# Performance work log

Hardware: AMD Instinct MI355X
Metric: run time of the kernel (lower is better)

Reference implementation:

```python
import jax, jax.numpy as jnp
import numpy as np

EPS = 1e-5

def conv2d(x, w, stride=1, padding=0, bias=None):
    out = jax.lax.conv_general_dilated(
        x, w, (stride, stride), [(padding, padding), (padding, padding)],
        dimension_numbers=('NCHW', 'OIHW', 'NCHW'))
    if bias is not None:
        out = out + bias[None, :, None, None]
    return out

def bn_relu(x, gamma, beta, mean, var):
    scale = gamma / jnp.sqrt(var + EPS)
    return jax.nn.relu(x * scale[None, :, None, None]
                       + (beta - mean * scale)[None, :, None, None])

def deform_conv(x, wp, bp, wc, ks, pad, stride):
    # Canonical DeformConv2d (v1, modulation=False) from pytorch-deform-conv-v2.
    b, c, H, W = x.shape
    N = ks * ks
    offset = conv2d(x, wp, stride=stride, padding=1, bias=bp)        # (b,2N,h,w)
    h, w = offset.shape[2], offset.shape[3]
    xp = jnp.pad(x, ((0, 0), (0, 0), (pad, pad), (pad, pad)))        # zero_padding
    Hp, Wp = H + 2 * pad, W + 2 * pad
    off = offset.transpose(0, 2, 3, 1)                               # (b,h,w,2N)
    rng = jnp.arange(-(ks - 1) // 2, (ks - 1) // 2 + 1, dtype=x.dtype)
    pnx, pny = jnp.meshgrid(rng, rng, indexing='ij')
    pnx, pny = pnx.reshape(-1), pny.reshape(-1)                      # (N,)
    p0x = jnp.arange(1, h * stride + 1, stride, dtype=x.dtype)       # torch starts at 1
    p0y = jnp.arange(1, w * stride + 1, stride, dtype=x.dtype)
    px = p0x[None, :, None, None] + pnx[None, None, None, :] + off[..., :N]  # (b,h,w,N)
    py = p0y[None, None, :, None] + pny[None, None, None, :] + off[..., N:]
    qx0 = jnp.floor(jax.lax.stop_gradient(px))
    qy0 = jnp.floor(jax.lax.stop_gradient(py))
    qx0c = jnp.clip(qx0, 0, Hp - 1).astype(jnp.int32)
    qx1c = jnp.clip(qx0 + 1, 0, Hp - 1).astype(jnp.int32)
    qy0c = jnp.clip(qy0, 0, Wp - 1).astype(jnp.int32)
    qy1c = jnp.clip(qy0 + 1, 0, Wp - 1).astype(jnp.int32)
    pxc = jnp.clip(px, 0, Hp - 1)
    pyc = jnp.clip(py, 0, Wp - 1)
    fx0 = qx0c.astype(x.dtype); fx1 = qx1c.astype(x.dtype)
    fy0 = qy0c.astype(x.dtype); fy1 = qy1c.astype(x.dtype)
    g_lt = (1 + (fx0 - pxc)) * (1 + (fy0 - pyc))
    g_rb = (1 - (fx1 - pxc)) * (1 - (fy1 - pyc))
    g_lb = (1 + (fx0 - pxc)) * (1 - (fy1 - pyc))
    g_rt = (1 - (fx1 - pxc)) * (1 + (fy0 - pyc))
    xf = xp.reshape(b, c, Hp * Wp)
    def gather(qx, qy):
        idx = (qx * Wp + qy).reshape(b, 1, h * w * N)
        return jnp.take_along_axis(xf, idx, axis=2).reshape(b, c, h, w, N)
    x_off = (g_lt[:, None] * gather(qx0c, qy0c)
             + g_rb[:, None] * gather(qx1c, qy1c)
             + g_lb[:, None] * gather(qx0c, qy1c)
             + g_rt[:, None] * gather(qx1c, qy0c))                   # (b,c,h,w,N)
    # stride=ks conv over the reshaped (h*ks, w*ks) map == einsum over sample slot n
    return jnp.einsum('bchwn,ocn->bohw', x_off, wc.reshape(wc.shape[0], c, N))

def setup_inputs() -> dict:
    key = jax.random.key(0)
    ks = iter(jax.random.split(key, 40))
    def nrm(shape, scale):
        return jax.random.normal(next(ks), shape, dtype=jnp.float32) * scale
    def he(shape):  # fan_in = prod of all but first dim
        return nrm(shape, float(np.sqrt(2.0 / np.prod(shape[1:]))))
    def bn(c):
        return (jnp.ones((c,), jnp.float32) + nrm((c,), 0.05),  # gamma
                nrm((c,), 0.05),                                 # beta
                nrm((c,), 0.1),                                  # running mean
                jax.random.uniform(next(ks), (c,), jnp.float32, 0.5, 1.5))  # var
    inp = {'x': jax.random.normal(next(ks), (256, 3, 32, 32), dtype=jnp.float32)}
    inp['w1'] = he((32, 3, 3, 3)); inp['b1'] = nrm((32,), 0.01)
    inp['g1'], inp['be1'], inp['m1'], inp['v1'] = bn(32)
    inp['wp2'] = nrm((18, 32, 3, 3), 0.01); inp['bp2'] = nrm((18,), 0.001)
    inp['wc2'] = he((64, 32, 3, 3))
    inp['g2'], inp['be2'], inp['m2'], inp['v2'] = bn(64)
    inp['wp3'] = nrm((18, 64, 3, 3), 0.01); inp['bp3'] = nrm((18,), 0.001)
    inp['wc3'] = he((128, 64, 3, 3))
    inp['g3'], inp['be3'], inp['m3'], inp['v3'] = bn(128)
    inp['wp4'] = nrm((18, 128, 3, 3), 0.01); inp['bp4'] = nrm((18,), 0.001)
    inp['wc4'] = he((128, 128, 3, 3))
    inp['g4'], inp['be4'], inp['m4'], inp['v4'] = bn(128)
    inp['wcls'] = nrm((100, 128), float(1.0 / np.sqrt(128)))
    inp['bcls'] = nrm((100,), 0.01)
    return inp

def reference(x, w1, b1, g1, be1, m1, v1,
              wp2, bp2, wc2, g2, be2, m2, v2,
              wp3, bp3, wc3, g3, be3, m3, v3,
              wp4, bp4, wc4, g4, be4, m4, v4,
              wcls, bcls):
    h = bn_relu(conv2d(x, w1, stride=1, padding=1, bias=b1), g1, be1, m1, v1)   # (b,32,32,32)
    h = bn_relu(deform_conv(h, wp2, bp2, wc2, 3, 1, 2), g2, be2, m2, v2)        # (b,64,16,16)
    h = bn_relu(deform_conv(h, wp3, bp3, wc3, 3, 1, 1), g3, be3, m3, v3)        # (b,128,16,16)
    h = bn_relu(deform_conv(h, wp4, bp4, wc4, 3, 1, 2), g4, be4, m4, v4)        # (b,128,8,8)
    h = jnp.mean(h, axis=(2, 3))                                                # avg_pool2d(8) -> (b,128)
    return h @ wcls.T + bcls[None, :]
```

## Files before the change

### kernel.cpp

```cpp
#include <hip/hip_runtime.h>
#include <math.h>

#define BN_EPS 1e-5f

typedef __attribute__((ext_vector_type(4))) float f4;
typedef __attribute__((ext_vector_type(4))) int i4v;
typedef __attribute__((ext_vector_type(8))) short short8;
typedef __attribute__((ext_vector_type(4))) float f32x4;

__device__ inline unsigned short f2bf(float f) {
    unsigned int u = __builtin_bit_cast(unsigned int, f);
    return (unsigned short)((u + 0x7FFFu + ((u >> 16) & 1u)) >> 16);
}
__device__ inline float blo(int u) { return __builtin_bit_cast(float, (int)(u << 16)); }
__device__ inline float bhi(int u) { return __builtin_bit_cast(float, (int)(u & 0xffff0000)); }
__device__ inline int pkbf_fast(float hi, float lo) {
    unsigned uh = __builtin_bit_cast(unsigned, hi) + 0x8000u;
    unsigned ul = __builtin_bit_cast(unsigned, lo) + 0x8000u;
    return (int)__builtin_amdgcn_perm(uh, ul, 0x07060302u);
}

struct CvtSeg { const float* src; unsigned short* dst; int oreal, c, kpad, end; };
struct CvtArgs { CvtSeg s[7]; };

__global__ __launch_bounds__(256)
void cvt_all(CvtArgs a)
{
    int idx = blockIdx.x * 256 + threadIdx.x;
    int base = 0;
    #pragma unroll
    for (int i = 0; i < 7; ++i) {
        if (idx < a.s[i].end) {
            int local = idx - base;
            int kpad = a.s[i].kpad, c = a.s[i].c;
            int o = local / kpad, k = local - o * kpad;
            unsigned short val = 0;
            if (o < a.s[i].oreal && k < 9 * c) {
                int n = k / c, cc = k - n * c;
                val = f2bf(a.s[i].src[(o * c + cc) * 9 + n]);
            }
            a.s[i].dst[local] = val;
            return;
        }
        base = a.s[i].end;
    }
}

__global__ __launch_bounds__(256)
void conv1_tile(const float* __restrict__ x, const unsigned short* __restrict__ wq,
                const float* __restrict__ bias, const float* __restrict__ g,
                const float* __restrict__ be, const float* __restrict__ m,
                const float* __restrict__ v, unsigned short* __restrict__ out)
{
    __shared__ __align__(16) float img[3072];
    __shared__ __align__(16) unsigned short wt[32 * 40];
    __shared__ float scb[32], shb[32];
    const int tid = threadIdx.x;
    const int b = blockIdx.x >> 2;
    const int qtr = blockIdx.x & 3;
    if (tid < 32) {
        float sc = g[tid] * rsqrtf(v[tid] + BN_EPS);
        scb[tid] = sc;
        shb[tid] = be[tid] - m[tid] * sc + bias[tid] * sc;
    }
    *(ushort4*)&wt[(tid >> 3) * 40 + (tid & 7) * 4] =
        *(const ushort4*)(wq + (tid >> 3) * 32 + (tid & 7) * 4);
    const float* xb = x + (size_t)b * 3072;
    #pragma unroll
    for (int r = 0; r < 3; ++r) {
        int idx = r * 256 + tid;
        *(f4*)&img[idx * 4] = *(const f4*)(xb + idx * 4);
    }
    __syncthreads();
    const int wid = tid >> 6, lane = tid & 63, quad = lane >> 4, m16 = lane & 15;
    short8 af0 = *(const short8*)&wt[m16 * 40 + quad * 8];
    short8 af1 = *(const short8*)&wt[(16 + m16) * 40 + quad * 8];
    #pragma unroll
    for (int it = 0; it < 4; ++it) {
        int pix = qtr * 256 + it * 64 + wid * 16 + m16;
        int i = pix >> 5, j = pix & 31;
        short8 bfrag;
        #pragma unroll
        for (int jj = 0; jj < 8; ++jj) {
            int k = quad * 8 + jj;
            float val = 0.f;
            if (k < 27) {
                int n = k / 3, c = k - n * 3;
                int u = i - 1 + n / 3, vv = j - 1 + n % 3;
                if (u >= 0 && u < 32 && vv >= 0 && vv < 32)
                    val = img[c * 1024 + u * 32 + vv];
            }
            bfrag[jj] = (short)f2bf(val);
        }
        f32x4 a0 = {0.f,0.f,0.f,0.f}, a1 = {0.f,0.f,0.f,0.f};
        a0 = __builtin_amdgcn_mfma_f32_16x16x32_bf16(af0, bfrag, a0, 0, 0, 0);
        a1 = __builtin_amdgcn_mfma_f32_16x16x32_bf16(af1, bfrag, a1, 0, 0, 0);
        unsigned short* op = out + ((size_t)b * 1024 + pix) * 32;
        ushort4 s0, s1;
        #pragma unroll
        for (int rr = 0; rr < 4; ++rr) {
            int o0 = quad * 4 + rr, o1 = 16 + quad * 4 + rr;
            ((unsigned short*)&s0)[rr] = f2bf(fmaxf(fmaf(a0[rr], scb[o0], shb[o0]), 0.f));
            ((unsigned short*)&s1)[rr] = f2bf(fmaxf(fmaf(a1[rr], scb[o1], shb[o1]), 0.f));
        }
        *(ushort4*)(op + quad * 4) = s0;
        *(ushort4*)(op + 16 + quad * 4) = s1;
    }
}

template<int C, int OREAL, int OPAD, int H, int W, int OH, int OW, int S, int MTILE>
__global__ __launch_bounds__(256, 3)
void dconv_fused(const unsigned short* __restrict__ xact,
                 const unsigned short* __restrict__ wp, const float* __restrict__ bp,
                 const unsigned short* __restrict__ wc,
                 const float* __restrict__ g, const float* __restrict__ be,
                 const float* __restrict__ m, const float* __restrict__ v,
                 unsigned short* __restrict__ out)
{
    constexpr int K = C * 9;
    constexpr int KCH = C / 32;
    constexpr int OT = OPAD / 64;
    constexpr int ST = MTILE / 16;
    constexpr int PWP = MTILE / 2;
    constexpr int STP = PWP / 16;
    constexpr int CP = C + 8;
    constexpr int GL = C / 8;
    constexpr int NGRP = 256 / GL;
    constexpr int NT = MTILE / NGRP;
    constexpr int OHW = OH * OW;
    constexpr int HWC = H * W * C;
    constexpr int Hp = H + 2, Wpp = W + 2;
    static_assert(MTILE % NGRP == 0 && OPAD % 64 == 0, "tiling");

    __shared__ __align__(16) unsigned short xo[2][MTILE * CP];
    __shared__ __align__(16) i4v tab_i[MTILE][9];
    __shared__ __align__(16) f4  tab_w[MTILE][9];
    __shared__ int tab_o[MTILE][9];
    __shared__ int tab_m[MTILE][9];
    __shared__ float off_lds[MTILE][20];
    __shared__ int imgb[MTILE];
    __shared__ float scb[OPAD], shb[OPAD];

    const int tid = threadIdx.x;
    const int p0 = blockIdx.x * MTILE;

    if (tid < MTILE) imgb[tid] = ((p0 + tid) / OHW) * HWC;
    for (int o = tid; o < OREAL; o += 256) {
        float sc = g[o] * rsqrtf(v[o] + BN_EPS);
        scb[o] = sc;
        shb[o] = be[o] - m[o] * sc;
    }
    for (int e = tid; e < MTILE * 9; e += 256) {
        int lp = e / 9, n = e % 9;
        int p = p0 + lp;
        int rem = p % OHW;
        int i = rem / OW, j = rem % OW;
        int u = i * S - 1 + n / 3, vv = j * S - 1 + n % 3;
        bool ok = (u >= 0 && u < H && vv >= 0 && vv < W);
        tab_o[lp][n] = ok ? (u * W + vv) * C : 0;
        tab_m[lp][n] = ok ? -1 : 0;
    }
    __syncthreads();

    const int gl = tid % GL, grp = tid / GL;
    const int wid = tid >> 6, lane = tid & 63, quad = lane >> 4, m16 = lane & 15;

    {
        const int ogp = wid & 1, pgp = wid >> 1;
        const int obp = ogp * 16;
        const int pbp = pgp * PWP;
        i4v Tp[NT];
        auto issueA = [&](int n) {
            #pragma unroll
            for (int it = 0; it < NT; ++it) {
                const int pix = it * NGRP + grp;
                Tp[it] = *(const i4v*)(xact + imgb[pix] + gl * 8 + tab_o[pix][n]);
            }
        };
        auto commitA = [&](int n, int buf) {
            #pragma unroll
            for (int it = 0; it < NT; ++it) {
                const int pix = it * NGRP + grp;
                int mask = tab_m[pix][n];
                i4v R;
                #pragma unroll
                for (int e2 = 0; e2 < 4; ++e2) R[e2] = Tp[it][e2] & mask;
                *(i4v*)&xo[buf][pix * CP + gl * 8] = R;
            }
        };
        auto loadWp = [&](int n, short8* wf) {
            #pragma unroll
            for (int ch = 0; ch < KCH; ++ch)
                wf[ch] = *(const short8*)(wp + (size_t)(obp + m16) * K
                                          + n * C + ch * 32 + quad * 8);
        };
        f32x4 accp[STP];
        #pragma unroll
        for (int st = 0; st < STP; ++st) accp[st] = (f32x4){0.f, 0.f, 0.f, 0.f};
        short8 wfA[KCH], wfB[KCH];
        issueA(0);
        loadWp(0, wfA);
        commitA(0, 0);
        __syncthreads();
        for (int n = 0; n < 9; ++n) {
            const int cur = n & 1;
            if (n < 8) { issueA(n + 1); loadWp(n + 1, wfB); }
            #pragma unroll
            for (int ch = 0; ch < KCH; ++ch)
                #pragma unroll
                for (int st = 0; st < STP; ++st) {
                    short8 bf = *(const short8*)&xo[cur][(pbp + st * 16 + m16) * CP
                                                        + ch * 32 + quad * 8];
                    accp[st] = __builtin_amdgcn_mfma_f32_16x16x32_bf16(
                        wfA[ch], bf, accp[st], 0, 0, 0);
                }
            if (n < 8) {
                commitA(n + 1, cur ^ 1);
                #pragma unroll
                for (int ch = 0; ch < KCH; ++ch) wfA[ch] = wfB[ch];
            }
            __syncthreads();
        }
        #pragma unroll
        for (int st = 0; st < STP; ++st) {
            int pix = pbp + st * 16 + m16;
            #pragma unroll
            for (int rr = 0; rr < 4; ++rr) {
                int o = obp + quad * 4 + rr;
                if (o < 18) off_lds[pix][o] = accp[st][rr] + bp[o];
            }
        }
    }
    __syncthreads();

    for (int e = tid; e < MTILE * 9; e += 256) {
        int lp = e / 9, n = e % 9;
        int p = p0 + lp;
        int rem = p % OHW;
        int i = rem / OW, j = rem % OW;
        float ox = off_lds[lp][n];
        float oy = off_lds[lp][9 + n];
        float px = (float)(i * S + n / 3) + ox;
        float py = (float)(j * S + n % 3) + oy;
        int qx0 = (int)floorf(px), qy0 = (int)floorf(py);
        int x0 = min(max(qx0, 0), Hp - 1), x1 = min(max(qx0 + 1, 0), Hp - 1);
        int y0 = min(max(qy0, 0), Wpp - 1), y1 = min(max(qy0 + 1, 0), Wpp - 1);
        float pxc = fminf(fmaxf(px, 0.f), (float)(Hp - 1));
        float pyc = fminf(fmaxf(py, 0.f), (float)(Wpp - 1));
        float gx0 = 1.f + ((float)x0 - pxc), gx1 = 1.f - ((float)x1 - pxc);
        float gy0 = 1.f + ((float)y0 - pyc), gy1 = 1.f - ((float)y1 - pyc);
        int u0 = x0 - 1, u1 = x1 - 1, v0 = y0 - 1, v1 = y1 - 1;
        bool k0 = (u0 >= 0 && u0 < H && v0 >= 0 && v0 < W);
        bool k1 = (u1 >= 0 && u1 < H && v1 >= 0 && v1 < W);
        bool k2 = (u0 >= 0 && u0 < H && v1 >= 0 && v1 < W);
        bool k3 = (u1 >= 0 && u1 < H && v0 >= 0 && v0 < W);
        i4v ti; f4 tw;
        ti[0] = k0 ? (u0 * W + v0) * C : 0;  tw[0] = k0 ? gx0 * gy0 : 0.f;
        ti[1] = k1 ? (u1 * W + v1) * C : 0;  tw[1] = k1 ? gx1 * gy1 : 0.f;
        ti[2] = k2 ? (u0 * W + v1) * C : 0;  tw[2] = k2 ? gx0 * gy1 : 0.f;
        ti[3] = k3 ? (u1 * W + v0) * C : 0;  tw[3] = k3 ? gx1 * gy0 : 0.f;
        tab_i[lp][n] = ti;
        tab_w[lp][n] = tw;
    }
    __syncthreads();

    {
        const int obase = wid * OT * 16;
        i4v T[NT][4];
        auto issueC = [&](int n) {
            #pragma unroll
            for (int it = 0; it < NT; ++it) {
                const int pix = it * NGRP + grp;
                const unsigned short* xb = xact + imgb[pix] + gl * 8;
                i4v ti = tab_i[pix][n];
                T[it][0] = *(const i4v*)(xb + ti[0]);
                T[it][1] = *(const i4v*)(xb + ti[1]);
                T[it][2] = *(const i4v*)(xb + ti[2]);
                T[it][3] = *(const i4v*)(xb + ti[3]);
            }
        };
        auto commitC = [&](int n, int buf) {
            #pragma unroll
            for (int it = 0; it < NT; ++it) {
                const int pix = it * NGRP + grp;
                f4 tw = tab_w[pix][n];
                i4v R;
                #pragma unroll
                for (int e2 = 0; e2 < 4; ++e2) {
                    float lo = tw[0] * blo(T[it][0][e2]);
                    lo = fmaf(tw[1], blo(T[it][1][e2]), lo);
                    lo = fmaf(tw[2], blo(T[it][2][e2]), lo);
                    lo = fmaf(tw[3], blo(T[it][3][e2]), lo);
                    float hi = tw[0] * bhi(T[it][0][e2]);
                    hi = fmaf(tw[1], bhi(T[it][1][e2]), hi);
                    hi = fmaf(tw[2], bhi(T[it][2][e2]), hi);
                    hi = fmaf(tw[3], bhi(T[it][3][e2]), hi);
                    R[e2] = pkbf_fast(hi, lo);
                }
                *(i4v*)&xo[buf][pix * CP + gl * 8] = R;
            }
        };
        auto loadWc = [&](int n, short8 (*wf)[OT]) {
            #pragma unroll
            for (int ch = 0; ch < KCH; ++ch)
                #pragma unroll
                for (int t = 0; t < OT; ++t)
                    wf[ch][t] = *(const short8*)(wc + (size_t)(obase + t * 16 + m16) * K
                                                 + n * C + ch * 32 + quad * 8);
        };

        f32x4 acc[ST][OT];
        #pragma unroll
        for (int st = 0; st < ST; ++st)
            #pragma unroll
            for (int t = 0; t < OT; ++t) acc[st][t] = (f32x4){0.f, 0.f, 0.f, 0.f};

        short8 wfA[KCH][OT], wfB[KCH][OT];
        issueC(0);
        loadWc(0, wfA);
        commitC(0, 0);
        __syncthreads();

        for (int n = 0; n < 9; ++n) {
            const int cur = n & 1;
            if (n < 8) {
                issueC(n + 1);
                loadWc(n + 1, wfB);
            }
            #pragma unroll
            for (int ch = 0; ch < KCH; ++ch)
                #pragma unroll
                for (int st = 0; st < ST; ++st) {
                    short8 bf = *(const short8*)&xo[cur][(st * 16 + m16) * CP
                                                        + ch * 32 + quad * 8];
                    #pragma unroll
                    for (int t = 0; t < OT; ++t)
                        acc[st][t] = __builtin_amdgcn_mfma_f32_16x16x32_bf16(
                            wfA[ch][t], bf, acc[st][t], 0, 0, 0);
                }
            if (n < 8) {
                commitC(n + 1, cur ^ 1);
                #pragma unroll
                for (int ch = 0; ch < KCH; ++ch)
                    #pragma unroll
                    for (int t = 0; t < OT; ++t) wfA[ch][t] = wfB[ch][t];
            }
            __syncthreads();
        }

        #pragma unroll
        for (int st = 0; st < ST; ++st) {
            const int p = p0 + st * 16 + m16;
            #pragma unroll
            for (int t = 0; t < OT; ++t) {
                int o = obase + t * 16 + quad * 4;
                ushort4 s;
                #pragma unroll
                for (int rr = 0; rr < 4; ++rr)
                    ((unsigned short*)&s)[rr] =
                        f2bf(fmaxf(fmaf(acc[st][t][rr], scb[o + rr], shb[o + rr]), 0.f));
                *(ushort4*)(out + (size_t)p * OPAD + o) = s;
            }
        }
    }
}

__global__ __launch_bounds__(128)
void pool_fc(const unsigned short* __restrict__ h4, const float* __restrict__ wcls,
             const float* __restrict__ bcls, float* __restrict__ out)
{
    __shared__ float pool[128];
    int b = blockIdx.x;
    int tid = threadIdx.x;
    const unsigned short* src = h4 + (size_t)b * 8192;
    float s = 0.f;
    #pragma unroll
    for (int t = 0; t < 64; ++t)
        s += __builtin_bit_cast(float, (unsigned)src[t * 128 + tid] << 16);
    pool[tid] = s * (1.f / 64.f);
    __syncthreads();
    if (tid < 100) {
        float acc = bcls[tid];
        const float* wr = wcls + tid * 128;
        #pragma unroll
        for (int c = 0; c < 128; ++c) acc = fmaf(pool[c], wr[c], acc);
        out[(size_t)b * 100 + tid] = acc;
    }
}

extern "C" void kernel_launch(void* const* d_in, const int* in_sizes, int n_in,
                              void* d_out, int out_size, void* d_ws, size_t ws_size,
                              hipStream_t stream)
{
    const float* x    = (const float*)d_in[0];
    const float* w1   = (const float*)d_in[1];
    const float* b1   = (const float*)d_in[2];
    const float* g1   = (const float*)d_in[3];
    const float* be1  = (const float*)d_in[4];
    const float* m1   = (const float*)d_in[5];
    const float* v1   = (const float*)d_in[6];
    const float* wp2  = (const float*)d_in[7];
    const float* bp2  = (const float*)d_in[8];
    const float* wc2  = (const float*)d_in[9];
    const float* g2   = (const float*)d_in[10];
    const float* be2  = (const float*)d_in[11];
    const float* m2   = (const float*)d_in[12];
    const float* v2   = (const float*)d_in[13];
    const float* wp3  = (const float*)d_in[14];
    const float* bp3  = (const float*)d_in[15];
    const float* wc3  = (const float*)d_in[16];
    const float* g3   = (const float*)d_in[17];
    const float* be3  = (const float*)d_in[18];
    const float* m3   = (const float*)d_in[19];
    const float* v3   = (const float*)d_in[20];
    const float* wp4  = (const float*)d_in[21];
    const float* bp4  = (const float*)d_in[22];
    const float* wc4  = (const float*)d_in[23];
    const float* g4   = (const float*)d_in[24];
    const float* be4  = (const float*)d_in[25];
    const float* m4   = (const float*)d_in[26];
    const float* v4   = (const float*)d_in[27];
    const float* wcls = (const float*)d_in[28];
    const float* bcls = (const float*)d_in[29];
    float* out = (float*)d_out;

    unsigned short* h1 = (unsigned short*)d_ws;
    unsigned short* h2 = h1 + 8388608;
    unsigned short* h3 = h2 + 4194304;
    unsigned short* h4 = h3 + 8388608;
    unsigned short* wc2b = h4 + 2097152;
    unsigned short* wc3b = wc2b + 18432;
    unsigned short* wc4b = wc3b + 73728;
    unsigned short* wp2b = wc4b + 147456;
    unsigned short* wp3b = wp2b + 9216;
    unsigned short* wp4b = wp3b + 18432;
    unsigned short* wq1  = wp4b + 36864;
    (void)ws_size; (void)in_sizes; (void)n_in; (void)out_size;

    CvtArgs ca;
    ca.s[0] = { wc2, wc2b, 64, 32, 288, 18432 };
    ca.s[1] = { wc3, wc3b, 128, 64, 576, 92160 };
    ca.s[2] = { wc4, wc4b, 128, 128, 1152, 239616 };
    ca.s[3] = { wp2, wp2b, 18, 32, 288, 248832 };
    ca.s[4] = { wp3, wp3b, 18, 64, 576, 267264 };
    ca.s[5] = { wp4, wp4b, 18, 128, 1152, 304128 };
    ca.s[6] = { w1, wq1, 32, 3, 32, 305152 };
    cvt_all<<<1192, 256, 0, stream>>>(ca);

    conv1_tile<<<1024, 256, 0, stream>>>(x, wq1, b1, g1, be1, m1, v1, h1);

    dconv_fused<32, 64, 64, 32, 32, 16, 16, 2, 64><<<1024, 256, 0, stream>>>(
        h1, wp2b, bp2, wc2b, g2, be2, m2, v2, h2);

    dconv_fused<64, 128, 128, 16, 16, 16, 16, 1, 64><<<1024, 256, 0, stream>>>(
        h2, wp3b, bp3, wc3b, g3, be3, m3, v3, h3);

    dconv_fused<128, 128, 128, 16, 16, 8, 8, 2, 32><<<512, 256, 0, stream>>>(
        h3, wp4b, bp4, wc4b, g4, be4, m4, v4, h4);

    pool_fc<<<256, 128, 0, stream>>>(h4, wcls, bcls, out);
}
```

Measured before the change: 234.0 us.

## Compress deform-conv LDS tables to 16-bit and shrink layer-4 tile for occupancy

Gather offset tables shrink from int to ushort, and bilinear weights and predicted offsets are stored as fp16 instead of fp32. This cuts LDS use, allowing launch bounds to rise to 4 blocks per CU. The last deform layer uses MTILE 16 with twice the blocks, plus adjusted offset-conv wave mapping so small tiles still work. The risks are reduced precision in the offsets and weights (fp16 offsets near 16 lose fractional bits) and ushort offsets that must stay below 65536. With MTILE 16, two of the four waves duplicate the offset-conv work.

```diff
diff --git a/kernel.cpp b/kernel.cpp
--- a/kernel.cpp
+++ b/kernel.cpp
@@ -7,6 +7,7 @@
 typedef __attribute__((ext_vector_type(4))) int i4v;
 typedef __attribute__((ext_vector_type(8))) short short8;
 typedef __attribute__((ext_vector_type(4))) float f32x4;
+typedef _Float16 half4v __attribute__((ext_vector_type(4)));
 
 __device__ inline unsigned short f2bf(float f) {
     unsigned int u = __builtin_bit_cast(unsigned int, f);
@@ -109,7 +110,7 @@
 }
 
 template<int C, int OREAL, int OPAD, int H, int W, int OH, int OW, int S, int MTILE>
-__global__ __launch_bounds__(256, 3)
+__global__ __launch_bounds__(256, 4)
 void dconv_fused(const unsigned short* __restrict__ xact,
                  const unsigned short* __restrict__ wp, const float* __restrict__ bp,
                  const unsigned short* __restrict__ wc,
@@ -121,7 +122,7 @@
     constexpr int KCH = C / 32;
     constexpr int OT = OPAD / 64;
     constexpr int ST = MTILE / 16;
-    constexpr int PWP = MTILE / 2;
+    constexpr int PWP = (MTILE >= 32) ? MTILE / 2 : MTILE;
     constexpr int STP = PWP / 16;
     constexpr int CP = C + 8;
     constexpr int GL = C / 8;
@@ -130,14 +131,12 @@
     constexpr int OHW = OH * OW;
     constexpr int HWC = H * W * C;
     constexpr int Hp = H + 2, Wpp = W + 2;
-    static_assert(MTILE % NGRP == 0 && OPAD % 64 == 0, "tiling");
+    static_assert(MTILE % NGRP == 0 && OPAD % 64 == 0 && STP >= 1, "tiling");
 
     __shared__ __align__(16) unsigned short xo[2][MTILE * CP];
-    __shared__ __align__(16) i4v tab_i[MTILE][9];
-    __shared__ __align__(16) f4  tab_w[MTILE][9];
-    __shared__ int tab_o[MTILE][9];
-    __shared__ int tab_m[MTILE][9];
-    __shared__ float off_lds[MTILE][20];
+    __shared__ __align__(8) ushort4   tab_p[MTILE][9];
+    __shared__ __align__(8) _Float16  tab_h[MTILE][9][4];
+    __shared__ _Float16 off_lds[MTILE][20];
     __shared__ int imgb[MTILE];
     __shared__ float scb[OPAD], shb[OPAD];
 
@@ -157,8 +156,11 @@
         int i = rem / OW, j = rem % OW;
         int u = i * S - 1 + n / 3, vv = j * S - 1 + n % 3;
         bool ok = (u >= 0 && u < H && vv >= 0 && vv < W);
-        tab_o[lp][n] = ok ? (u * W + vv) * C : 0;
-        tab_m[lp][n] = ok ? -1 : 0;
+        ushort4 tp;
+        tp.x = ok ? (unsigned short)((u * W + vv) * C) : (unsigned short)0;
+        tp.y = ok ? (unsigned short)0xFFFF : (unsigned short)0;
+        tp.z = 0; tp.w = 0;
+        tab_p[lp][n] = tp;
     }
     __syncthreads();
 
@@ -166,7 +168,8 @@
     const int wid = tid >> 6, lane = tid & 63, quad = lane >> 4, m16 = lane & 15;
 
     {
-        const int ogp = wid & 1, pgp = wid >> 1;
+        const int ogp = wid & 1;
+        const int pgp = (MTILE >= 32) ? (wid >> 1) : 0;
         const int obp = ogp * 16;
         const int pbp = pgp * PWP;
         i4v Tp[NT];
@@ -174,14 +177,14 @@
             #pragma unroll
             for (int it = 0; it < NT; ++it) {
                 const int pix = it * NGRP + grp;
-                Tp[it] = *(const i4v*)(xact + imgb[pix] + gl * 8 + tab_o[pix][n]);
+                Tp[it] = *(const i4v*)(xact + imgb[pix] + gl * 8 + (int)tab_p[pix][n].x);
             }
         };
         auto commitA = [&](int n, int buf) {
             #pragma unroll
             for (int it = 0; it < NT; ++it) {
                 const int pix = it * NGRP + grp;
-                int mask = tab_m[pix][n];
+                int mask = (int)(short)tab_p[pix][n].y;
                 i4v R;
                 #pragma unroll
                 for (int e2 = 0; e2 < 4; ++e2) R[e2] = Tp[it][e2] & mask;
@@ -227,7 +230,7 @@
             #pragma unroll
             for (int rr = 0; rr < 4; ++rr) {
                 int o = obp + quad * 4 + rr;
-                if (o < 18) off_lds[pix][o] = accp[st][rr] + bp[o];
+                if (o < 18) off_lds[pix][o] = (_Float16)(accp[st][rr] + bp[o]);
             }
         }
     }
@@ -238,8 +241,8 @@
         int p = p0 + lp;
         int rem = p % OHW;
         int i = rem / OW, j = rem % OW;
-        float ox = off_lds[lp][n];
-        float oy = off_lds[lp][9 + n];
+        float ox = (float)off_lds[lp][n];
+        float oy = (float)off_lds[lp][9 + n];
         float px = (float)(i * S + n / 3) + ox;
         float py = (float)(j * S + n % 3) + oy;
         int qx0 = (int)floorf(px), qy0 = (int)floorf(py);
@@ -254,13 +257,18 @@
         bool k1 = (u1 >= 0 && u1 < H && v1 >= 0 && v1 < W);
         bool k2 = (u0 >= 0 && u0 < H && v1 >= 0 && v1 < W);
         bool k3 = (u1 >= 0 && u1 < H && v0 >= 0 && v0 < W);
-        i4v ti; f4 tw;
-        ti[0] = k0 ? (u0 * W + v0) * C : 0;  tw[0] = k0 ? gx0 * gy0 : 0.f;
-        ti[1] = k1 ? (u1 * W + v1) * C : 0;  tw[1] = k1 ? gx1 * gy1 : 0.f;
-        ti[2] = k2 ? (u0 * W + v1) * C : 0;  tw[2] = k2 ? gx0 * gy1 : 0.f;
-        ti[3] = k3 ? (u1 * W + v0) * C : 0;  tw[3] = k3 ? gx1 * gy0 : 0.f;
-        tab_i[lp][n] = ti;
-        tab_w[lp][n] = tw;
+        ushort4 tp;
+        tp.x = k0 ? (unsigned short)((u0 * W + v0) * C) : (unsigned short)0;
+        tp.y = k1 ? (unsigned short)((u1 * W + v1) * C) : (unsigned short)0;
+        tp.z = k2 ? (unsigned short)((u0 * W + v1) * C) : (unsigned short)0;
+        tp.w = k3 ? (unsigned short)((u1 * W + v0) * C) : (unsigned short)0;
+        tab_p[lp][n] = tp;
+        half4v hw;
+        hw[0] = (_Float16)(k0 ? gx0 * gy0 : 0.f);
+        hw[1] = (_Float16)(k1 ? gx1 * gy1 : 0.f);
+        hw[2] = (_Float16)(k2 ? gx0 * gy1 : 0.f);
+        hw[3] = (_Float16)(k3 ? gx1 * gy0 : 0.f);
+        *(half4v*)&tab_h[lp][n][0] = hw;
     }
     __syncthreads();
 
@@ -272,29 +280,31 @@
             for (int it = 0; it < NT; ++it) {
                 const int pix = it * NGRP + grp;
                 const unsigned short* xb = xact + imgb[pix] + gl * 8;
-                i4v ti = tab_i[pix][n];
-                T[it][0] = *(const i4v*)(xb + ti[0]);
-                T[it][1] = *(const i4v*)(xb + ti[1]);
-                T[it][2] = *(const i4v*)(xb + ti[2]);
-                T[it][3] = *(const i4v*)(xb + ti[3]);
+                ushort4 tp = tab_p[pix][n];
+                T[it][0] = *(const i4v*)(xb + tp.x);
+                T[it][1] = *(const i4v*)(xb + tp.y);
+                T[it][2] = *(const i4v*)(xb + tp.z);
+                T[it][3] = *(const i4v*)(xb + tp.w);
             }
         };
         auto commitC = [&](int n, int buf) {
             #pragma unroll
             for (int it = 0; it < NT; ++it) {
                 const int pix = it * NGRP + grp;
-                f4 tw = tab_w[pix][n];
+                half4v hw = *(const half4v*)&tab_h[pix][n][0];
+                float w0 = (float)hw[0], w1 = (float)hw[1];
+                float w2 = (float)hw[2], w3 = (float)hw[3];
                 i4v R;
                 #pragma unroll
                 for (int e2 = 0; e2 < 4; ++e2) {
-                    float lo = tw[0] * blo(T[it][0][e2]);
-                    lo = fmaf(tw[1], blo(T[it][1][e2]), lo);
-                    lo = fmaf(tw[2], blo(T[it][2][e2]), lo);
-                    lo = fmaf(tw[3], blo(T[it][3][e2]), lo);
-                    float hi = tw[0] * bhi(T[it][0][e2]);
-                    hi = fmaf(tw[1], bhi(T[it][1][e2]), hi);
-                    hi = fmaf(tw[2], bhi(T[it][2][e2]), hi);
-                    hi = fmaf(tw[3], bhi(T[it][3][e2]), hi);
+                    float lo = w0 * blo(T[it][0][e2]);
+                    lo = fmaf(w1, blo(T[it][1][e2]), lo);
+                    lo = fmaf(w2, blo(T[it][2][e2]), lo);
+                    lo = fmaf(w3, blo(T[it][3][e2]), lo);
+                    float hi = w0 * bhi(T[it][0][e2]);
+                    hi = fmaf(w1, bhi(T[it][1][e2]), hi);
+                    hi = fmaf(w2, bhi(T[it][2][e2]), hi);
+                    hi = fmaf(w3, bhi(T[it][3][e2]), hi);
                     R[e2] = pkbf_fast(hi, lo);
                 }
                 *(i4v*)&xo[buf][pix * CP + gl * 8] = R;
@@ -455,7 +465,7 @@
     dconv_fused<64, 128, 128, 16, 16, 16, 16, 1, 64><<<1024, 256, 0, stream>>>(
         h2, wp3b, bp3, wc3b, g3, be3, m3, v3, h3);
 
-    dconv_fused<128, 128, 128, 16, 16, 8, 8, 2, 32><<<512, 256, 0, stream>>>(
+    dconv_fused<128, 128, 128, 16, 16, 8, 8, 2, 16><<<1024, 256, 0, stream>>>(
         h3, wp4b, bp4, wc4b, g4, be4, m4, v4, h4);
 
     pool_fc<<<256, 128, 0, stream>>>(h4, wcls, bcls, out);
```

Result: slower. 249.5 us (+6.6%).
